# Kernel tuning notes

Hardware: AMD Instinct MI355X
Metric: run time of the kernel (lower is better)

## Reference

```python
import jax, jax.numpy as jnp
import numpy as np

N = 10000
E = 320000

def gcn_layer(x, W, edge_src, edge_dst, edge_weight):
    # support = x @ W ; out = spmm(adj, support) via edge-list scatter-add
    support = x @ W                                  # [N, H]
    msgs = edge_weight[:, None] * support[edge_src]  # [E, H] gather (irregular)
    return jax.ops.segment_sum(msgs, edge_dst, num_segments=N)

def setup_inputs() -> dict:
    key = jax.random.key(0)
    ks = jax.random.split(key, 7)
    F_in, H1, H2 = 3000, 512, 64
    x = jax.random.normal(ks[0], (N, F_in), dtype=jnp.float32)
    edge_src = jax.random.randint(ks[1], (E,), 0, N)
    edge_dst = jax.random.randint(ks[2], (E,), 0, N)
    edge_weight = jax.random.uniform(ks[3], (E,), dtype=jnp.float32)
    W1 = jax.random.normal(ks[4], (F_in, H1), dtype=jnp.float32) * (1.0 / np.sqrt(F_in))
    W2 = jax.random.normal(ks[5], (H1, H2), dtype=jnp.float32) * (1.0 / np.sqrt(H1))
    W3 = jax.random.normal(ks[6], (H1, H2), dtype=jnp.float32) * (1.0 / np.sqrt(H1))
    return {"x": x, "edge_src": edge_src, "edge_dst": edge_dst,
            "edge_weight": edge_weight, "W1": W1, "W2": W2, "W3": W3}

def reference(x, edge_src, edge_dst, edge_weight, W1, W2, W3):
    # Eval mode: dropout is identity, reparameterize returns mu.
    h1 = jax.nn.relu(gcn_layer(x, W1, edge_src, edge_dst, edge_weight))  # [N, H1]
    mu = gcn_layer(h1, W2, edge_src, edge_dst, edge_weight)              # [N, H2]
    logvar = gcn_layer(h1, W3, edge_src, edge_dst, edge_weight)          # [N, H2]
    z = mu
    pred = z @ z.T  # InnerProductDecoder with act = identity -> [N, N]
    return (pred, mu, logvar)
```

## Files before the change

kernel.cpp:

```cpp
#include <hip/hip_runtime.h>
#include <hip/hip_bf16.h>

#define N_NODES 10000
#define N_EDGES 320000
#define F_IN    3000
#define KP      3008
#define H1      512
#define H2      64
#define CAP     128
#define NT      (KP / 32)

typedef float  f32x4  __attribute__((ext_vector_type(4)));
typedef short  bf16x8 __attribute__((ext_vector_type(8)));
typedef unsigned short us8 __attribute__((ext_vector_type(8)));

__device__ __forceinline__ unsigned short f2b(float f) {
    union { float f; unsigned u; } v; v.f = f;
    unsigned r = v.u + 0x7FFF + ((v.u >> 16) & 1);
    return (unsigned short)(r >> 16);
}
__device__ __forceinline__ float b2f(unsigned short b) {
    union { unsigned u; float f; } v; v.u = ((unsigned)b) << 16;
    return v.f;
}

#define GLOAD_LDS16(gptr, lptr)                                                             \
    __builtin_amdgcn_global_load_lds((const __attribute__((address_space(1))) void*)(gptr), \
                                     (__attribute__((address_space(3))) void*)(lptr),       \
                                     16, 0, 0)

#define NB_BUCKET 1250
#define NB_CONVX  14688
#define NB_CONVW  376

__global__ __launch_bounds__(256) void prep(const int* __restrict__ src,
                                            const int* __restrict__ dst,
                                            const float* __restrict__ w,
                                            const float* __restrict__ x,
                                            const float* __restrict__ W1,
                                            int* __restrict__ cnt,
                                            int* __restrict__ bsrc,
                                            float* __restrict__ bw,
                                            unsigned short* __restrict__ xb,
                                            unsigned short* __restrict__ w1t) {
    __shared__ float tr[64][65];
    const int b = blockIdx.x;
    const int t = threadIdx.x;
    if (b < NB_BUCKET) {
        int e = b * 256 + t;
        if (e >= N_EDGES) return;
        int d = dst[e];
        int slot = atomicAdd(&cnt[d], 1);
        if (slot < CAP) {
            bsrc[d * CAP + slot] = src[e];
            bw[d * CAP + slot]   = w[e];
        }
    } else if (b < NB_BUCKET + NB_CONVX) {
        int idx = (b - NB_BUCKET) * 256 + t;
        int r = idx / (KP / 8);
        int g = idx % (KP / 8);
        if (r >= N_NODES) return;
        us8 v;
        if (g * 8 + 8 <= F_IN) {
            float4 a = *(const float4*)&x[(size_t)r * F_IN + g * 8];
            float4 c = *(const float4*)&x[(size_t)r * F_IN + g * 8 + 4];
            v[0] = f2b(a.x); v[1] = f2b(a.y); v[2] = f2b(a.z); v[3] = f2b(a.w);
            v[4] = f2b(c.x); v[5] = f2b(c.y); v[6] = f2b(c.z); v[7] = f2b(c.w);
        } else {
            #pragma unroll
            for (int j = 0; j < 8; ++j) {
                int k = g * 8 + j;
                v[j] = (k < F_IN) ? f2b(x[(size_t)r * F_IN + k]) : (unsigned short)0;
            }
        }
        *(us8*)&xb[(size_t)r * KP + g * 8] = v;
    } else {
        int bb = b - NB_BUCKET - NB_CONVX;
        int kBase = (bb >> 3) * 64;
        int cBase = (bb & 7) * 64;
        int col = cBase + (t & 63);
        #pragma unroll
        for (int i = 0; i < 16; ++i) {
            int row = kBase + i * 4 + (t >> 6);
            float v = (row < F_IN) ? W1[(size_t)row * H1 + col] : 0.f;
            tr[t & 63][i * 4 + (t >> 6)] = v;
        }
        __syncthreads();
        int c = t >> 2, kq = (t & 3) * 16;
        us8 o0, o1;
        #pragma unroll
        for (int j = 0; j < 8; ++j) { o0[j] = f2b(tr[c][kq + j]); o1[j] = f2b(tr[c][kq + 8 + j]); }
        *(us8*)&w1t[(size_t)(cBase + c) * KP + kBase + kq]     = o0;
        *(us8*)&w1t[(size_t)(cBase + c) * KP + kBase + kq + 8] = o1;
    }
}

__global__ __launch_bounds__(256, 6) void gemm1_mfma(const unsigned short* __restrict__ xb,
                                                     const unsigned short* __restrict__ w1t,
                                                     unsigned short* __restrict__ Cb) {
    __shared__ unsigned short As[2][128 * 32];
    __shared__ unsigned short Bs[2][64 * 32];
    const int f  = blockIdx.x;
    const int k8 = f & 7;
    const int jj = f >> 3;
    const int bx = k8 * 10 + (jj >> 3);
    const int by = jj & 7;
    const int mBase = bx * 128;
    const int nBase = by * 64;

    const int t = threadIdx.x;
    const int wid = t >> 6, lane = t & 63;
    const int wr = (wid >> 1) * 64;
    const int wc = (wid & 1) * 32;
    const int fr = lane & 15;
    const int swz = (((lane >> 4) ^ (fr & 3)) << 3);

    const int srow   = lane >> 2;
    const int schunk = ((lane & 3) ^ (srow & 3)) * 8;
    const int arow0  = min(mBase + wid * 16 + srow, N_NODES - 1);
    const int arow1  = min(mBase + (wid + 4) * 16 + srow, N_NODES - 1);
    const int brow   = nBase + wid * 16 + srow;

    f32x4 acc[4][2] = {};

#define STAGE1(c, k0)                                                              \
    do {                                                                           \
        GLOAD_LDS16(&xb[(size_t)arow0 * KP + (k0) + schunk], &As[c][wid * 512]);   \
        GLOAD_LDS16(&xb[(size_t)arow1 * KP + (k0) + schunk], &As[c][(wid + 4) * 512]); \
        GLOAD_LDS16(&w1t[(size_t)brow * KP + (k0) + schunk], &Bs[c][wid * 512]);   \
    } while (0)

#define COMPUTE1(c)                                                            \
    do {                                                                       \
        bf16x8 af[4], bfv[2];                                                  \
        _Pragma("unroll")                                                      \
        for (int m = 0; m < 4; ++m)                                            \
            af[m] = *(const bf16x8*)&As[c][(wr + m * 16 + fr) * 32 + swz];     \
        _Pragma("unroll")                                                      \
        for (int n = 0; n < 2; ++n)                                            \
            bfv[n] = *(const bf16x8*)&Bs[c][(wc + n * 16 + fr) * 32 + swz];    \
        _Pragma("unroll")                                                      \
        for (int m = 0; m < 4; ++m)                                            \
            _Pragma("unroll")                                                  \
            for (int n = 0; n < 2; ++n)                                        \
                acc[m][n] = __builtin_amdgcn_mfma_f32_16x16x32_bf16(af[m], bfv[n], acc[m][n], 0, 0, 0); \
    } while (0)

    STAGE1(0, 0);
    __syncthreads();
    int cur = 0;
    for (int tt = 0; tt < NT - 1; ++tt) {
        STAGE1(cur ^ 1, (tt + 1) * 32);
        COMPUTE1(cur);
        __syncthreads();
        cur ^= 1;
    }
    COMPUTE1(cur);

#undef STAGE1
#undef COMPUTE1

    #pragma unroll
    for (int m = 0; m < 4; ++m) {
        int rbase = mBase + wr + m * 16 + (lane >> 4) * 4;
        #pragma unroll
        for (int n = 0; n < 2; ++n) {
            int col = nBase + wc + n * 16 + (lane & 15);
            #pragma unroll
            for (int i = 0; i < 4; ++i) {
                int row = rbase + i;
                if (row < N_NODES)
                    Cb[(size_t)row * H1 + col] = f2b(acc[m][n][i]);
            }
        }
    }
}

__global__ __launch_bounds__(512) void gather_gemm23(const unsigned short* __restrict__ sup,
                                                     const int* __restrict__ cnt,
                                                     const int* __restrict__ bsrc,
                                                     const float* __restrict__ bw,
                                                     const float* __restrict__ W2,
                                                     const float* __restrict__ W3,
                                                     float* __restrict__ sup2) {
    __shared__ float hs[16][H1];
    const int t = threadIdx.x;
    const int wid = t >> 6, lane = t & 63;
    const int rBase = blockIdx.x * 16;

    #pragma unroll
    for (int i = 0; i < 2; ++i) {
        const int local = wid * 2 + i;
        const int n = rBase + local;
        const int deg = min(cnt[n], CAP);
        float acc[8] = {};
        for (int e = 0; e < deg; ++e) {
            int   s = bsrc[n * CAP + e];
            float w = bw[n * CAP + e];
            us8 v = *(const us8*)&sup[(size_t)s * H1 + lane * 8];
            #pragma unroll
            for (int j = 0; j < 8; ++j) acc[j] += w * b2f(v[j]);
        }
        *(float4*)&hs[local][lane * 8] =
            make_float4(fmaxf(acc[0], 0.f), fmaxf(acc[1], 0.f), fmaxf(acc[2], 0.f), fmaxf(acc[3], 0.f));
        *(float4*)&hs[local][lane * 8 + 4] =
            make_float4(fmaxf(acc[4], 0.f), fmaxf(acc[5], 0.f), fmaxf(acc[6], 0.f), fmaxf(acc[7], 0.f));
    }
    __syncthreads();

    const int col = t & 127;
    const int rg  = (t >> 7) * 4;
    const float* W = (col < 64) ? (W2 + col) : (W3 + (col - 64));
    float acc2[4] = {};
    for (int k = 0; k < H1; ++k) {
        float wv = W[k * 64];
        #pragma unroll
        for (int i = 0; i < 4; ++i) acc2[i] += wv * hs[rg + i][k];
    }
    #pragma unroll
    for (int i = 0; i < 4; ++i)
        sup2[(size_t)(rBase + rg + i) * 128 + col] = acc2[i];
}

__global__ __launch_bounds__(256) void gather_muvar(const float* __restrict__ sup2,
                                                    const int* __restrict__ cnt,
                                                    const int* __restrict__ bsrc,
                                                    const float* __restrict__ bw,
                                                    float* __restrict__ mu,
                                                    float* __restrict__ lv,
                                                    unsigned short* __restrict__ mub) {
    const int n  = blockIdx.x * 8 + (threadIdx.x >> 5);
    const int c4 = (threadIdx.x & 31) * 4;
    const int deg = min(cnt[n], CAP);
    float4 acc = make_float4(0.f, 0.f, 0.f, 0.f);
    for (int e = 0; e < deg; ++e) {
        int   s = bsrc[n * CAP + e];
        float w = bw[n * CAP + e];
        float4 v = *(const float4*)&sup2[(size_t)s * 128 + c4];
        acc.x += w * v.x; acc.y += w * v.y; acc.z += w * v.z; acc.w += w * v.w;
    }
    if (c4 < 64) {
        *(float4*)&mu[(size_t)n * 64 + c4] = acc;
        mub[(size_t)n * 64 + c4 + 0] = f2b(acc.x);
        mub[(size_t)n * 64 + c4 + 1] = f2b(acc.y);
        mub[(size_t)n * 64 + c4 + 2] = f2b(acc.z);
        mub[(size_t)n * 64 + c4 + 3] = f2b(acc.w);
    } else {
        *(float4*)&lv[(size_t)n * 64 + (c4 - 64)] = acc;
    }
}

__global__ __launch_bounds__(256) void pred_mfma(const unsigned short* __restrict__ mub,
                                                 float* __restrict__ pred) {
    __shared__ float st[4][16][68];
    const int t = threadIdx.x, wid = t >> 6, lane = t & 63;
    const int rb = blockIdx.x * 128 + (wid >> 1) * 64;
    const int cb = blockIdx.y * 128 + (wid & 1) * 64;
    const int fr = lane & 15, fk = (lane >> 4) * 8;
    f32x4 acc[4][4] = {};

    #pragma unroll
    for (int ks = 0; ks < 2; ++ks) {
        bf16x8 af[4], bfv[4];
        #pragma unroll
        for (int m = 0; m < 4; ++m) {
            int r = min(rb + m * 16 + fr, N_NODES - 1);
            af[m] = *(const bf16x8*)&mub[(size_t)r * 64 + ks * 32 + fk];
        }
        #pragma unroll
        for (int n = 0; n < 4; ++n) {
            int c = min(cb + n * 16 + fr, N_NODES - 1);
            bfv[n] = *(const bf16x8*)&mub[(size_t)c * 64 + ks * 32 + fk];
        }
        #pragma unroll
        for (int m = 0; m < 4; ++m)
            #pragma unroll
            for (int n = 0; n < 4; ++n)
                acc[m][n] = __builtin_amdgcn_mfma_f32_16x16x32_bf16(af[m], bfv[n], acc[m][n], 0, 0, 0);
    }

    #pragma unroll
    for (int m = 0; m < 4; ++m) {
        #pragma unroll
        for (int n = 0; n < 4; ++n)
            #pragma unroll
            for (int i = 0; i < 4; ++i)
                st[wid][(lane >> 4) * 4 + i][n * 16 + (lane & 15)] = acc[m][n][i];
        int rbase = rb + m * 16;
        #pragma unroll
        for (int it = 0; it < 4; ++it) {
            int row   = it * 4 + (lane >> 4);
            int chunk = lane & 15;
            int grow  = rbase + row;
            int gcol  = cb + chunk * 4;
            if (grow < N_NODES) {
                f32x4 v = *(const f32x4*)&st[wid][row][chunk * 4];
                if (gcol + 3 < N_NODES) {
                    __builtin_nontemporal_store(v, (f32x4*)&pred[(size_t)grow * N_NODES + gcol]);
                } else {
                    #pragma unroll
                    for (int j = 0; j < 4; ++j)
                        if (gcol + j < N_NODES)
                            __builtin_nontemporal_store(v[j], &pred[(size_t)grow * N_NODES + gcol + j]);
                }
            }
        }
    }
}

extern "C" void kernel_launch(void* const* d_in, const int* in_sizes, int n_in,
                              void* d_out, int out_size, void* d_ws, size_t ws_size,
                              hipStream_t stream) {
    const float* x    = (const float*)d_in[0];
    const int*   esrc = (const int*)d_in[1];
    const int*   edst = (const int*)d_in[2];
    const float* ew   = (const float*)d_in[3];
    const float* W1   = (const float*)d_in[4];
    const float* W2   = (const float*)d_in[5];
    const float* W3   = (const float*)d_in[6];

    float* pred = (float*)d_out;
    float* mu   = pred + (size_t)N_NODES * N_NODES;
    float* lv   = mu   + (size_t)N_NODES * H2;

    char* ws = (char*)d_ws;
    unsigned short* sup1b = (unsigned short*)ws; ws += (size_t)N_NODES * H1 * sizeof(short);
    float* support2 = (float*)ws; ws += (size_t)N_NODES * 2 * H2 * sizeof(float);
    int*   cnt      = (int*)ws;   ws += (size_t)N_NODES * sizeof(int);
    int*   bsrc     = (int*)ws;   ws += (size_t)N_NODES * CAP * sizeof(int);
    float* bw       = (float*)ws; ws += (size_t)N_NODES * CAP * sizeof(float);
    unsigned short* xb  = (unsigned short*)ws; ws += (size_t)N_NODES * KP * sizeof(short);
    unsigned short* w1t = (unsigned short*)ws; ws += (size_t)H1 * KP * sizeof(short);
    unsigned short* mub = (unsigned short*)ws; ws += (size_t)N_NODES * H2 * sizeof(short);

    (void)hipMemsetAsync(cnt, 0, N_NODES * sizeof(int), stream);
    prep<<<NB_BUCKET + NB_CONVX + NB_CONVW, 256, 0, stream>>>(esrc, edst, ew, x, W1,
                                                              cnt, bsrc, bw, xb, w1t);
    gemm1_mfma<<<640, 256, 0, stream>>>(xb, w1t, sup1b);
    gather_gemm23<<<N_NODES / 16, 512, 0, stream>>>(sup1b, cnt, bsrc, bw, W2, W3, support2);
    gather_muvar<<<N_NODES / 8, 256, 0, stream>>>(support2, cnt, bsrc, bw, mu, lv, mub);
    pred_mfma<<<dim3((N_NODES + 127) / 128, (N_NODES + 127) / 128), 256, 0, stream>>>(mub, pred);
}
```

Before: 337.8 us.

## Store layer-2 support in bf16 and hand-tune GEMM1 pipeline barriers

The intermediate support2 buffer is now stored as bf16 instead of fp32. This halves the bytes gathered per edge in the mu/logvar aggregation, which now processes 16 nodes per block with 8-wide bf16 loads. Separately, the GEMM1 main loop replaces __syncthreads with explicit vmcnt/lgkmcnt waits, raw s_barrier and sched_barrier, so the prefetch of the next tile can overlap the MFMA compute. The bf16 intermediate adds rounding error to mu and logvar, and the manual waitcnt counts must match the number of loads STAGE1 issues to stay correct.

Measured after the change: 323.4 us. -4.3%, faster.

```diff
diff --git a/kernel.cpp b/kernel.cpp
--- a/kernel.cpp
+++ b/kernel.cpp
@@ -147,14 +147,20 @@
     } while (0)
 
     STAGE1(0, 0);
-    __syncthreads();
     int cur = 0;
     for (int tt = 0; tt < NT - 1; ++tt) {
         STAGE1(cur ^ 1, (tt + 1) * 32);
+        asm volatile("s_waitcnt vmcnt(3)" ::: "memory");
+        __builtin_amdgcn_s_barrier();
+        __builtin_amdgcn_sched_barrier(0);
         COMPUTE1(cur);
-        __syncthreads();
+        asm volatile("s_waitcnt lgkmcnt(0)" ::: "memory");
+        __builtin_amdgcn_sched_barrier(0);
+        __builtin_amdgcn_s_barrier();
         cur ^= 1;
     }
+    asm volatile("s_waitcnt vmcnt(0)" ::: "memory");
+    __builtin_amdgcn_s_barrier();
     COMPUTE1(cur);
 
 #undef STAGE1
@@ -182,7 +188,7 @@
                                                      const float* __restrict__ bw,
                                                      const float* __restrict__ W2,
                                                      const float* __restrict__ W3,
-                                                     float* __restrict__ sup2) {
+                                                     unsigned short* __restrict__ sup2b) {
     __shared__ float hs[16][H1];
     const int t = threadIdx.x;
     const int wid = t >> 6, lane = t & 63;
@@ -219,34 +225,37 @@
     }
     #pragma unroll
     for (int i = 0; i < 4; ++i)
-        sup2[(size_t)(rBase + rg + i) * 128 + col] = acc2[i];
-}
-
-__global__ __launch_bounds__(256) void gather_muvar(const float* __restrict__ sup2,
+        sup2b[(size_t)(rBase + rg + i) * 128 + col] = f2b(acc2[i]);
+}
+
+__global__ __launch_bounds__(256) void gather_muvar(const unsigned short* __restrict__ sup2b,
                                                     const int* __restrict__ cnt,
                                                     const int* __restrict__ bsrc,
                                                     const float* __restrict__ bw,
                                                     float* __restrict__ mu,
                                                     float* __restrict__ lv,
                                                     unsigned short* __restrict__ mub) {
-    const int n  = blockIdx.x * 8 + (threadIdx.x >> 5);
-    const int c4 = (threadIdx.x & 31) * 4;
+    const int n  = blockIdx.x * 16 + (threadIdx.x >> 4);
+    const int c8 = (threadIdx.x & 15) * 8;
     const int deg = min(cnt[n], CAP);
-    float4 acc = make_float4(0.f, 0.f, 0.f, 0.f);
+    float acc[8] = {};
     for (int e = 0; e < deg; ++e) {
         int   s = bsrc[n * CAP + e];
         float w = bw[n * CAP + e];
-        float4 v = *(const float4*)&sup2[(size_t)s * 128 + c4];
-        acc.x += w * v.x; acc.y += w * v.y; acc.z += w * v.z; acc.w += w * v.w;
-    }
-    if (c4 < 64) {
-        *(float4*)&mu[(size_t)n * 64 + c4] = acc;
-        mub[(size_t)n * 64 + c4 + 0] = f2b(acc.x);
-        mub[(size_t)n * 64 + c4 + 1] = f2b(acc.y);
-        mub[(size_t)n * 64 + c4 + 2] = f2b(acc.z);
-        mub[(size_t)n * 64 + c4 + 3] = f2b(acc.w);
+        us8 v = *(const us8*)&sup2b[(size_t)s * 128 + c8];
+        #pragma unroll
+        for (int j = 0; j < 8; ++j) acc[j] += w * b2f(v[j]);
+    }
+    if (c8 < 64) {
+        *(float4*)&mu[(size_t)n * 64 + c8]     = make_float4(acc[0], acc[1], acc[2], acc[3]);
+        *(float4*)&mu[(size_t)n * 64 + c8 + 4] = make_float4(acc[4], acc[5], acc[6], acc[7]);
+        us8 o;
+        #pragma unroll
+        for (int j = 0; j < 8; ++j) o[j] = f2b(acc[j]);
+        *(us8*)&mub[(size_t)n * 64 + c8] = o;
     } else {
-        *(float4*)&lv[(size_t)n * 64 + (c4 - 64)] = acc;
+        *(float4*)&lv[(size_t)n * 64 + (c8 - 64)]     = make_float4(acc[0], acc[1], acc[2], acc[3]);
+        *(float4*)&lv[(size_t)n * 64 + (c8 - 64) + 4] = make_float4(acc[4], acc[5], acc[6], acc[7]);
     }
 }
 
@@ -325,7 +334,7 @@
 
     char* ws = (char*)d_ws;
     unsigned short* sup1b = (unsigned short*)ws; ws += (size_t)N_NODES * H1 * sizeof(short);
-    float* support2 = (float*)ws; ws += (size_t)N_NODES * 2 * H2 * sizeof(float);
+    unsigned short* sup2b = (unsigned short*)ws; ws += (size_t)N_NODES * 2 * H2 * sizeof(short);
     int*   cnt      = (int*)ws;   ws += (size_t)N_NODES * sizeof(int);
     int*   bsrc     = (int*)ws;   ws += (size_t)N_NODES * CAP * sizeof(int);
     float* bw       = (float*)ws; ws += (size_t)N_NODES * CAP * sizeof(float);
@@ -337,7 +346,7 @@
     prep<<<NB_BUCKET + NB_CONVX + NB_CONVW, 256, 0, stream>>>(esrc, edst, ew, x, W1,
                                                               cnt, bsrc, bw, xb, w1t);
     gemm1_mfma<<<640, 256, 0, stream>>>(xb, w1t, sup1b);
-    gather_gemm23<<<N_NODES / 16, 512, 0, stream>>>(sup1b, cnt, bsrc, bw, W2, W3, support2);
-    gather_muvar<<<N_NODES / 8, 256, 0, stream>>>(support2, cnt, bsrc, bw, mu, lv, mub);
+    gather_gemm23<<<N_NODES / 16, 512, 0, stream>>>(sup1b, cnt, bsrc, bw, W2, W3, sup2b);
+    gather_muvar<<<N_NODES / 16, 256, 0, stream>>>(sup2b, cnt, bsrc, bw, mu, lv, mub);
     pred_mfma<<<dim3((N_NODES + 127) / 128, (N_NODES + 127) / 128), 256, 0, stream>>>(mub, pred);
 }
```
